# Performance work log

Measured on AMD Instinct MI355X. Metric: run time of the kernel, lower is better.

The kernel has to match this reference:

```python
import jax, jax.numpy as jnp
import numpy as np

VMIN, VMAX, N = -5.0, 5.0, 100          # InvertiblePWL defaults
INT_LEN = (VMAX - VMIN) / (N - 1)       # bin width
B, D = 2_000_000, 16


def setup_inputs() -> dict:
    key = jax.random.key(0)
    k1, k2, k3, k4 = jax.random.split(key, 4)
    eps = jax.random.normal(k1, (B, D), dtype=jnp.float32)
    # small-magnitude adjacency so (I - A) is well-conditioned
    A = 0.05 * jax.random.normal(k2, (D, D), dtype=jnp.float32)
    # per-dim PWL params: torch inits p = randn(n+1)/5, b = randn(1) + vmin
    p = jax.random.normal(k3, (D, N + 1), dtype=jnp.float32) / 5.0
    b = jax.random.normal(k4, (D,), dtype=jnp.float32) + VMIN
    return {"eps": eps, "A": A, "p": p, "b": b}


def _pwl_forward(z, p, b):
    """Vectorized InvertiblePWL.forward over all d dims at once.
    z: [B, d]; p: [d, N+1]; b: [d]  ->  out: [B, d]
    """
    points = jnp.linspace(VMIN, VMAX, N, dtype=z.dtype)  # [N], same for all dims
    # delta_h is detached in torch (p[1:n] slice) -> stop_gradient
    delta_h = jax.lax.stop_gradient(INT_LEN * (jnp.exp(p[:, 1:N]) + 0.001))  # [d, N-1]
    # serial cumsum in torch == prefix-sum: delta_bias[0]=b, delta_bias[i+1]=delta_bias[i]+delta_h[i]
    delta_bias = b[:, None] + jnp.concatenate(
        [jnp.zeros((p.shape[0], 1), z.dtype), jnp.cumsum(delta_h, axis=1)], axis=1
    )  # [d, N]
    # index = sum(eps >= points) == searchsorted(points, z, 'right'), in [0, N]
    index = jnp.searchsorted(points, z, side="right")          # [B, d]
    sp_idx = jnp.maximum(index - 1, 0)                          # clamp at 0
    db = jnp.take_along_axis(delta_bias.T, sp_idx, axis=0)      # [B, d]
    sp = jax.lax.stop_gradient(points[sp_idx])                  # start points, detached
    w = jnp.exp(jnp.take_along_axis(p.T, index, axis=0)) + 0.001  # [B, d]
    return (z - sp) * w + db


def reference(eps, A, p, b):
    d = A.shape[0]
    # SCM.inv_cal: z = eps @ inv(I - A)
    adj_normalized = jnp.linalg.inv(jnp.eye(d, dtype=A.dtype) - A)
    z = eps @ adj_normalized                                    # [B, d]
    # SCM.prior_nlr: per-dim InvertiblePWL
    return _pwl_forward(z, p, b)
```

## Files before the change

### kernel.cpp

```cpp
#include <hip/hip_runtime.h>
#include <math.h>

#define D_DIM 16
#define N_PTS 100
#define VMIN_F (-5.0f)
#define INT_LEN_F (10.0f / 99.0f)
#define INV_INT_LEN_F (99.0f / 10.0f)

__global__ void scm_setup(const float* __restrict__ A,
                          const float* __restrict__ p,
                          const float* __restrict__ b,
                          float* __restrict__ Minv,
                          float2* __restrict__ Ctab) {
    __shared__ double aug[16][33];
    __shared__ float db_s[16][N_PTS];
    __shared__ int piv;
    const int t = threadIdx.x;

    if (t < 16) {
        #pragma unroll
        for (int j = 0; j < 16; j++) {
            aug[t][j]      = (t == j ? 1.0 : 0.0) - (double)A[t * 16 + j];
            aug[t][16 + j] = (t == j ? 1.0 : 0.0);
        }
    }
    __syncthreads();

    for (int k = 0; k < 16; k++) {
        if (t == 0) {
            int pr = k; double best = fabs(aug[k][k]);
            for (int i = k + 1; i < 16; i++) {
                double v = fabs(aug[i][k]);
                if (v > best) { best = v; pr = i; }
            }
            piv = pr;
        }
        __syncthreads();
        const int pr = piv;
        if (pr != k && t < 32) {
            double tmp = aug[k][t]; aug[k][t] = aug[pr][t]; aug[pr][t] = tmp;
        }
        __syncthreads();
        const double pivval = aug[k][k];
        __syncthreads();
        if (t < 32) aug[k][t] = aug[k][t] / pivval;
        __syncthreads();
        if (t < 16 && t != k) {
            const double f = aug[t][k];
            #pragma unroll
            for (int j = 0; j < 32; j++) aug[t][j] -= f * aug[k][j];
        }
        __syncthreads();
    }

    if (t < 16) {
        #pragma unroll
        for (int j = 0; j < 16; j++) Minv[t * 16 + j] = (float)aug[t][16 + j];
    }

    if (t < 16) {
        float acc = b[t];
        db_s[t][0] = acc;
        for (int i = 1; i < N_PTS; i++) {
            acc += INT_LEN_F * (expf(p[t * (N_PTS + 1) + i]) + 0.001f);
            db_s[t][i] = acc;
        }
    }
    __syncthreads();

    for (int i = t; i < 16 * (N_PTS + 1); i += blockDim.x) {
        const int d   = i / (N_PTS + 1);
        const int idx = i - d * (N_PTS + 1);
        const int spi = idx > 0 ? idx - 1 : 0;
        float2 c;
        c.x = expf(p[i]) + 0.001f;
        c.y = db_s[d][spi];
        Ctab[i] = c;
    }
}

template <int J>
__device__ __forceinline__ float dpp_bcast(float x) {
    constexpr int ctrl = J | (J << 2) | (J << 4) | (J << 6);
    int xi = __builtin_bit_cast(int, x);
    int r  = __builtin_amdgcn_mov_dpp(xi, ctrl, 0xf, 0xf, true);
    return __builtin_bit_cast(float, r);
}

__global__ __launch_bounds__(256, 4) void scm_main(
        const float* __restrict__ eps,
        const float* __restrict__ Minv,
        const float2* __restrict__ Ctab,
        float* __restrict__ out, int B) {
    __shared__ float2 sC[16 * (N_PTS + 1)];

    const int t = threadIdx.x;
    const int q = t & 3;

    for (int i = t; i < 16 * (N_PTS + 1); i += 256) sC[i] = Ctab[i];

    float4 Mcol[16];
    #pragma unroll
    for (int k = 0; k < 16; k++)
        Mcol[k] = *(const float4*)(Minv + k * 16 + 4 * q);

    __syncthreads();

    const long total  = (long)B * 4;
    const long stride = (long)gridDim.x * 256;
    long f4 = (long)blockIdx.x * 256 + t;

    const float4* in4  = (const float4*)eps;
    float4*       out4 = (float4*)out;

    float4 cur = make_float4(0.f, 0.f, 0.f, 0.f);
    if (f4 < total) cur = in4[f4];

    for (; f4 < total; f4 += stride) {
        const long nf4 = f4 + stride;
        float4 nxt = make_float4(0.f, 0.f, 0.f, 0.f);
        if (nf4 < total) nxt = in4[nf4];

        float e[16];
        e[0]  = dpp_bcast<0>(cur.x); e[1]  = dpp_bcast<0>(cur.y);
        e[2]  = dpp_bcast<0>(cur.z); e[3]  = dpp_bcast<0>(cur.w);
        e[4]  = dpp_bcast<1>(cur.x); e[5]  = dpp_bcast<1>(cur.y);
        e[6]  = dpp_bcast<1>(cur.z); e[7]  = dpp_bcast<1>(cur.w);
        e[8]  = dpp_bcast<2>(cur.x); e[9]  = dpp_bcast<2>(cur.y);
        e[10] = dpp_bcast<2>(cur.z); e[11] = dpp_bcast<2>(cur.w);
        e[12] = dpp_bcast<3>(cur.x); e[13] = dpp_bcast<3>(cur.y);
        e[14] = dpp_bcast<3>(cur.z); e[15] = dpp_bcast<3>(cur.w);

        float z0 = 0.f, z1 = 0.f, z2 = 0.f, z3 = 0.f;
        #pragma unroll
        for (int k = 0; k < 16; k++) {
            z0 = fmaf(e[k], Mcol[k].x, z0);
            z1 = fmaf(e[k], Mcol[k].y, z1);
            z2 = fmaf(e[k], Mcol[k].z, z2);
            z3 = fmaf(e[k], Mcol[k].w, z3);
        }

        float zv[4] = {z0, z1, z2, z3};
        float o[4];
        #pragma unroll
        for (int i = 0; i < 4; i++) {
            const float zd = zv[i];
            const float tt = (zd - VMIN_F) * INV_INT_LEN_F;
            int idx = (int)floorf(tt) + 1;
            idx = min(max(idx, 0), N_PTS);
            const int sp_idx = max(idx - 1, 0);
            const float sp = VMIN_F + (float)sp_idx * INT_LEN_F;
            const float2 c = sC[(4 * q + i) * (N_PTS + 1) + idx];
            o[i] = fmaf(zd - sp, c.x, c.y);
        }

        out4[f4] = make_float4(o[0], o[1], o[2], o[3]);
        cur = nxt;
    }
}

extern "C" void kernel_launch(void* const* d_in, const int* in_sizes, int n_in,
                              void* d_out, int out_size, void* d_ws, size_t ws_size,
                              hipStream_t stream) {
    const float* eps = (const float*)d_in[0];
    const float* A   = (const float*)d_in[1];
    const float* p   = (const float*)d_in[2];
    const float* b   = (const float*)d_in[3];
    float* out = (float*)d_out;

    const int B = in_sizes[0] / D_DIM;

    float*  ws   = (float*)d_ws;
    float*  Minv = ws;
    float2* Ctab = (float2*)(ws + 256);

    scm_setup<<<1, 256, 0, stream>>>(A, p, b, Minv, Ctab);

    long total_f4 = (long)B * 4;
    int blocks = (int)((total_f4 + 255) / 256);
    if (blocks > 2048) blocks = 2048;
    if (blocks < 1) blocks = 1;
    scm_main<<<blocks, 256, 0, stream>>>(eps, Minv, Ctab, out, B);
}
```

Measured before the change: 271.0 us.

## Unroll grid-stride loop by four, move matrix to LDS, use nontemporal stores

The main loop now handles four float4 rows per thread per iteration, and the next four are prefetched so more global loads are in flight. The inverse matrix columns move from 64 registers into shared memory and are read once per k step, shared across the four rows, which frees registers. Output writes use nontemporal stores to avoid polluting the cache, and index arithmetic drops from 64-bit to 32-bit. The cost is more LDS reads and larger live state for the prefetched data.

```diff
diff --git a/kernel.cpp b/kernel.cpp
--- a/kernel.cpp
+++ b/kernel.cpp
@@ -6,6 +6,9 @@
 #define VMIN_F (-5.0f)
 #define INT_LEN_F (10.0f / 99.0f)
 #define INV_INT_LEN_F (99.0f / 10.0f)
+#define UF 4
+
+typedef float f32x4_t __attribute__((ext_vector_type(4)));
 
 __global__ void scm_setup(const float* __restrict__ A,
                           const float* __restrict__ p,
@@ -93,69 +96,93 @@
         const float2* __restrict__ Ctab,
         float* __restrict__ out, int B) {
     __shared__ float2 sC[16 * (N_PTS + 1)];
+    __shared__ float4 sM[64];
 
     const int t = threadIdx.x;
     const int q = t & 3;
 
     for (int i = t; i < 16 * (N_PTS + 1); i += 256) sC[i] = Ctab[i];
-
-    float4 Mcol[16];
-    #pragma unroll
-    for (int k = 0; k < 16; k++)
-        Mcol[k] = *(const float4*)(Minv + k * 16 + 4 * q);
-
+    ((float*)sM)[t] = Minv[t];
     __syncthreads();
 
-    const long total  = (long)B * 4;
-    const long stride = (long)gridDim.x * 256;
-    long f4 = (long)blockIdx.x * 256 + t;
+    const float4* sMq = sM + q;
+
+    const int total  = B * 4;
+    const int stride = (int)gridDim.x * 256;
+    const int sstep  = stride * UF;
+    int base = (int)blockIdx.x * 256 + t;
 
     const float4* in4  = (const float4*)eps;
     float4*       out4 = (float4*)out;
 
-    float4 cur = make_float4(0.f, 0.f, 0.f, 0.f);
-    if (f4 < total) cur = in4[f4];
-
-    for (; f4 < total; f4 += stride) {
-        const long nf4 = f4 + stride;
-        float4 nxt = make_float4(0.f, 0.f, 0.f, 0.f);
-        if (nf4 < total) nxt = in4[nf4];
-
-        float e[16];
-        e[0]  = dpp_bcast<0>(cur.x); e[1]  = dpp_bcast<0>(cur.y);
-        e[2]  = dpp_bcast<0>(cur.z); e[3]  = dpp_bcast<0>(cur.w);
-        e[4]  = dpp_bcast<1>(cur.x); e[5]  = dpp_bcast<1>(cur.y);
-        e[6]  = dpp_bcast<1>(cur.z); e[7]  = dpp_bcast<1>(cur.w);
-        e[8]  = dpp_bcast<2>(cur.x); e[9]  = dpp_bcast<2>(cur.y);
-        e[10] = dpp_bcast<2>(cur.z); e[11] = dpp_bcast<2>(cur.w);
-        e[12] = dpp_bcast<3>(cur.x); e[13] = dpp_bcast<3>(cur.y);
-        e[14] = dpp_bcast<3>(cur.z); e[15] = dpp_bcast<3>(cur.w);
-
-        float z0 = 0.f, z1 = 0.f, z2 = 0.f, z3 = 0.f;
-        #pragma unroll
-        for (int k = 0; k < 16; k++) {
-            z0 = fmaf(e[k], Mcol[k].x, z0);
-            z1 = fmaf(e[k], Mcol[k].y, z1);
-            z2 = fmaf(e[k], Mcol[k].z, z2);
-            z3 = fmaf(e[k], Mcol[k].w, z3);
-        }
-
-        float zv[4] = {z0, z1, z2, z3};
-        float o[4];
-        #pragma unroll
-        for (int i = 0; i < 4; i++) {
-            const float zd = zv[i];
-            const float tt = (zd - VMIN_F) * INV_INT_LEN_F;
-            int idx = (int)floorf(tt) + 1;
-            idx = min(max(idx, 0), N_PTS);
-            const int sp_idx = max(idx - 1, 0);
-            const float sp = VMIN_F + (float)sp_idx * INT_LEN_F;
-            const float2 c = sC[(4 * q + i) * (N_PTS + 1) + idx];
-            o[i] = fmaf(zd - sp, c.x, c.y);
-        }
-
-        out4[f4] = make_float4(o[0], o[1], o[2], o[3]);
-        cur = nxt;
+    float4 cur[UF];
+    #pragma unroll
+    for (int u = 0; u < UF; u++) {
+        const int idx = base + u * stride;
+        cur[u] = (idx < total) ? in4[idx] : make_float4(0.f, 0.f, 0.f, 0.f);
+    }
+
+    for (; base < total; base += sstep) {
+        const int nbase = base + sstep;
+        float4 nxt[UF];
+        #pragma unroll
+        for (int u = 0; u < UF; u++) {
+            const int idx = nbase + u * stride;
+            nxt[u] = (idx < total) ? in4[idx] : make_float4(0.f, 0.f, 0.f, 0.f);
+        }
+
+        float4 z0 = make_float4(0.f, 0.f, 0.f, 0.f);
+        float4 z1 = make_float4(0.f, 0.f, 0.f, 0.f);
+        float4 z2 = make_float4(0.f, 0.f, 0.f, 0.f);
+        float4 z3 = make_float4(0.f, 0.f, 0.f, 0.f);
+
+#define SCM_STEP(G, C, COMP)                                                   \
+        {                                                                      \
+            const float4 mk = sMq[4 * (4 * (G) + (C))];                        \
+            const float e0 = dpp_bcast<(G)>(cur[0].COMP);                      \
+            const float e1 = dpp_bcast<(G)>(cur[1].COMP);                      \
+            const float e2 = dpp_bcast<(G)>(cur[2].COMP);                      \
+            const float e3 = dpp_bcast<(G)>(cur[3].COMP);                      \
+            z0.x = fmaf(e0, mk.x, z0.x); z0.y = fmaf(e0, mk.y, z0.y);          \
+            z0.z = fmaf(e0, mk.z, z0.z); z0.w = fmaf(e0, mk.w, z0.w);          \
+            z1.x = fmaf(e1, mk.x, z1.x); z1.y = fmaf(e1, mk.y, z1.y);          \
+            z1.z = fmaf(e1, mk.z, z1.z); z1.w = fmaf(e1, mk.w, z1.w);          \
+            z2.x = fmaf(e2, mk.x, z2.x); z2.y = fmaf(e2, mk.y, z2.y);          \
+            z2.z = fmaf(e2, mk.z, z2.z); z2.w = fmaf(e2, mk.w, z2.w);          \
+            z3.x = fmaf(e3, mk.x, z3.x); z3.y = fmaf(e3, mk.y, z3.y);          \
+            z3.z = fmaf(e3, mk.z, z3.z); z3.w = fmaf(e3, mk.w, z3.w);          \
+        }
+        SCM_STEP(0, 0, x) SCM_STEP(0, 1, y) SCM_STEP(0, 2, z) SCM_STEP(0, 3, w)
+        SCM_STEP(1, 0, x) SCM_STEP(1, 1, y) SCM_STEP(1, 2, z) SCM_STEP(1, 3, w)
+        SCM_STEP(2, 0, x) SCM_STEP(2, 1, y) SCM_STEP(2, 2, z) SCM_STEP(2, 3, w)
+        SCM_STEP(3, 0, x) SCM_STEP(3, 1, y) SCM_STEP(3, 2, z) SCM_STEP(3, 3, w)
+#undef SCM_STEP
+
+        float4 zarr[UF] = {z0, z1, z2, z3};
+        #pragma unroll
+        for (int u = 0; u < UF; u++) {
+            const int idx = base + u * stride;
+            const float zv[4] = {zarr[u].x, zarr[u].y, zarr[u].z, zarr[u].w};
+            float o[4];
+            #pragma unroll
+            for (int i = 0; i < 4; i++) {
+                const float zd = zv[i];
+                const float tt = (zd - VMIN_F) * INV_INT_LEN_F;
+                int id = (int)floorf(tt) + 1;
+                id = min(max(id, 0), N_PTS);
+                const int sp_idx = max(id - 1, 0);
+                const float sp = VMIN_F + (float)sp_idx * INT_LEN_F;
+                const float2 c = sC[(4 * q + i) * (N_PTS + 1) + id];
+                o[i] = fmaf(zd - sp, c.x, c.y);
+            }
+            if (idx < total) {
+                const f32x4_t v = {o[0], o[1], o[2], o[3]};
+                __builtin_nontemporal_store(v, (f32x4_t*)(out4 + idx));
+            }
+        }
+
+        #pragma unroll
+        for (int u = 0; u < UF; u++) cur[u] = nxt[u];
     }
 }
 
```

New measurement: 496.8 us. 83.3% more time.
